# Performance work log

Hardware: AMD Instinct MI355X
Metric: run time of the kernel (lower is better)

Reference implementation:

```python
import jax, jax.numpy as jnp
import numpy as np

B, N, C, K, D, H = 4, 16000, 128, 16, 4, 512
EPS = 1e-5


def _bn(x, g, b, m, v):
    # eval-mode BatchNorm1d over channel dim (applied to flattened B*N rows)
    return (x - m) * jax.lax.rsqrt(v + EPS) * g + b


def _ffn(x, W1, b1, W2, g, b, m, v):
    h = jax.nn.gelu(jnp.einsum('bnc,ch->bnh', x, W1) + b1)
    y = jnp.einsum('bnh,hc->bnc', h, W2)  # second linear has no bias
    return _bn(y, g, b, m, v)


def _vector_feature(x, knn):
    # knn edge max-pooling: max_k ( x[b, knn[b,n,k], :] - x[b, n, :] )
    gathered = jnp.take_along_axis(x[:, :, None, :], knn[:, :, :, None], axis=1)  # (B,N,K,C)
    return jnp.max(gathered - x[:, :, None, :], axis=2)


def _vfr(x, knn, W, g, b, m, v):
    y = jnp.einsum('bnc,cd->bnd', x, W)
    y = _vector_feature(y, knn)
    return _bn(y, g, b, m, v)


def setup_inputs():
    key = jax.random.key(0)
    ks = jax.random.split(key, 16)
    s = 0.05
    return {
        'x': jax.random.normal(ks[0], (B, N, C), jnp.float32),
        'pe': jax.random.normal(ks[1], (B, N, C), jnp.float32),
        'knn': jax.random.randint(ks[2], (B, N, K), 0, N, dtype=jnp.int32),
        # mlp (the single leading FFN)
        'mlp_W1': jax.random.normal(ks[3], (C, H), jnp.float32) * s,
        'mlp_b1': jnp.zeros((H,), jnp.float32),
        'mlp_W2': jax.random.normal(ks[4], (H, C), jnp.float32) * s,
        'mlp_g': jax.random.uniform(ks[5], (C,), jnp.float32, 0.5, 1.5),
        'mlp_beta': jnp.zeros((C,), jnp.float32),
        'mlp_m': jnp.zeros((C,), jnp.float32),
        'mlp_v': jnp.ones((C,), jnp.float32),
        # per-depth VFR params (stacked over depth D)
        'vfr_W': jax.random.normal(ks[6], (D, C, C), jnp.float32) * s,
        'vfr_g': jax.random.uniform(ks[7], (D, C), jnp.float32, 0.5, 1.5),
        'vfr_beta': jnp.zeros((D, C), jnp.float32),
        'vfr_m': jnp.zeros((D, C), jnp.float32),
        'vfr_v': jnp.ones((D, C), jnp.float32),
        # per-depth FFN params
        'ffn_W1': jax.random.normal(ks[8], (D, C, H), jnp.float32) * s,
        'ffn_b1': jnp.zeros((D, H), jnp.float32),
        'ffn_W2': jax.random.normal(ks[9], (D, H, C), jnp.float32) * s,
        'ffn_g': jax.random.uniform(ks[10], (D, C), jnp.float32, 0.5, 1.5),
        'ffn_beta': jnp.zeros((D, C), jnp.float32),
        'ffn_m': jnp.zeros((D, C), jnp.float32),
        'ffn_v': jnp.ones((D, C), jnp.float32),
    }


def reference(x, pe, knn,
              mlp_W1, mlp_b1, mlp_W2, mlp_g, mlp_beta, mlp_m, mlp_v,
              vfr_W, vfr_g, vfr_beta, vfr_m, vfr_v,
              ffn_W1, ffn_b1, ffn_W2, ffn_g, ffn_beta, ffn_m, ffn_v):
    # drop_path is identity in eval mode
    x = x + _ffn(x, mlp_W1, mlp_b1, mlp_W2, mlp_g, mlp_beta, mlp_m, mlp_v)
    for i in range(D):
        x = x + pe
        x = x + _vfr(x, knn, vfr_W[i], vfr_g[i], vfr_beta[i], vfr_m[i], vfr_v[i])
        x = x + _ffn(x, ffn_W1[i], ffn_b1[i], ffn_W2[i], ffn_g[i], ffn_beta[i], ffn_m[i], ffn_v[i])
    return x
```

## Files before the change

kernel.cpp:

```cpp
#include <hip/hip_runtime.h>
#include <hip/hip_bf16.h>

typedef __attribute__((ext_vector_type(8))) short bf16x8;
typedef __attribute__((ext_vector_type(4))) float f32x4;

#define B_ 4
#define N_ 16000
#define C_ 128
#define K_ 16
#define D_ 4
#define H_ 512
#define R_ (B_*N_)
#define TM 64
#define EPSV 1e-5f

__device__ __forceinline__ ushort f2bf(float f) {
    uint32_t b = __builtin_bit_cast(uint32_t, f);
    b += 0x7fffu + ((b >> 16) & 1u);
    return (ushort)(b >> 16);
}
__device__ __forceinline__ float bf2f(ushort u) {
    return __builtin_bit_cast(float, (uint32_t)u << 16);
}
__device__ __forceinline__ float gelu_fast(float v) {
    float v2 = v * v;
    float u = v * fmaf(0.0356774081f, v2, 0.7978845608f);
    float e = __expf(-2.0f * u);
    return v * __builtin_amdgcn_rcpf(1.0f + e);
}
__device__ __forceinline__ void gll16(const void* g, void* l) {
    __builtin_amdgcn_global_load_lds(
        (__attribute__((address_space(1))) void*)g,
        (__attribute__((address_space(3))) void*)l, 16, 0, 0);
}

__global__ void prep_kernel(
    const float* __restrict__ mlp_W1, const float* __restrict__ mlp_b1,
    const float* __restrict__ mlp_W2, const float* __restrict__ mlp_g,
    const float* __restrict__ mlp_be, const float* __restrict__ mlp_m,
    const float* __restrict__ mlp_v,
    const float* __restrict__ vfr_W, const float* __restrict__ vfr_g,
    const float* __restrict__ vfr_be, const float* __restrict__ vfr_m,
    const float* __restrict__ vfr_v,
    const float* __restrict__ ffn_W1, const float* __restrict__ ffn_b1,
    const float* __restrict__ ffn_W2, const float* __restrict__ ffn_g,
    const float* __restrict__ ffn_be, const float* __restrict__ ffn_m,
    const float* __restrict__ ffn_v,
    ushort* __restrict__ w1t, ushort* __restrict__ w2t, ushort* __restrict__ wvt,
    float* __restrict__ b1a, float* __restrict__ fs, float* __restrict__ fb,
    float* __restrict__ vs, float* __restrict__ vb)
{
    int i = blockIdx.x * 256 + threadIdx.x;
    const int NW = 5 * H_ * C_;
    if (i < NW) {
        int f = i / (H_*C_), e = i % (H_*C_);
        int h = e / C_, c = e % C_;
        const float* src = (f == 0) ? mlp_W1 : ffn_W1 + (size_t)(f-1)*C_*H_;
        w1t[i] = f2bf(src[(size_t)c*H_ + h]);
        return;
    }
    i -= NW;
    if (i < NW) {
        int f = i / (H_*C_), e = i % (H_*C_);
        int c = e / H_, h = e % H_;
        const float* src = (f == 0) ? mlp_W2 : ffn_W2 + (size_t)(f-1)*H_*C_;
        w2t[i] = f2bf(src[(size_t)h*C_ + c]);
        return;
    }
    i -= NW;
    if (i < D_*C_*C_) {
        int d = i / (C_*C_), e = i % (C_*C_);
        int co = e / C_, k = e % C_;
        wvt[i] = f2bf(vfr_W[(size_t)d*C_*C_ + (size_t)k*C_ + co]);
        return;
    }
    i -= D_*C_*C_;
    if (i < 5*H_) {
        int f = i / H_, h = i % H_;
        b1a[i] = (f == 0) ? mlp_b1[h] : ffn_b1[(f-1)*H_ + h];
        return;
    }
    i -= 5*H_;
    if (i < 5*C_) {
        int f = i / C_, c = i % C_;
        float g  = (f==0) ? mlp_g[c]  : ffn_g[(f-1)*C_ + c];
        float be = (f==0) ? mlp_be[c] : ffn_be[(f-1)*C_ + c];
        float m  = (f==0) ? mlp_m[c]  : ffn_m[(f-1)*C_ + c];
        float v  = (f==0) ? mlp_v[c]  : ffn_v[(f-1)*C_ + c];
        float s = g * rsqrtf(v + EPSV);
        fs[i] = s; fb[i] = be - m * s;
        return;
    }
    i -= 5*C_;
    if (i < D_*C_) {
        float s = vfr_g[i] * rsqrtf(vfr_v[i] + EPSV);
        vs[i] = s; vb[i] = vfr_be[i] - vfr_m[i] * s;
    }
}

__global__ __launch_bounds__(256, 4) void ffn_kernel(
    const float* __restrict__ xin, float* __restrict__ xout,
    const ushort* __restrict__ W1t,
    const ushort* __restrict__ W2t,
    const float* __restrict__ b1,
    const float* __restrict__ bns, const float* __restrict__ bnb)
{
    __shared__ __attribute__((aligned(16))) char lds[16384 + 16384 + 8192];
    char* W1s = lds;
    char* W2s = lds + 16384;
    char* Hs  = lds + 32768;

    const int tid  = threadIdx.x;
    const int m0   = blockIdx.x * TM;
    const int wv   = tid >> 6;
    const int lane = tid & 63;
    const int lr   = lane & 15;
    const int lh   = lane >> 4;

    bf16x8 xa[4];
    {
        const float* xrow = xin + (size_t)(m0 + wv*16 + lr) * C_ + lh*8;
        #pragma unroll
        for (int kk = 0; kk < 4; ++kk) {
            float4 v0 = *(const float4*)(xrow + kk*32);
            float4 v1 = *(const float4*)(xrow + kk*32 + 4);
            bf16x8 pk;
            pk[0]=(short)f2bf(v0.x); pk[1]=(short)f2bf(v0.y);
            pk[2]=(short)f2bf(v0.z); pk[3]=(short)f2bf(v0.w);
            pk[4]=(short)f2bf(v1.x); pk[5]=(short)f2bf(v1.y);
            pk[6]=(short)f2bf(v1.z); pk[7]=(short)f2bf(v1.w);
            xa[kk] = pk;
        }
    }

    f32x4 acc2[8];
    #pragma unroll
    for (int i = 0; i < 8; ++i) acc2[i] = (f32x4){0.f,0.f,0.f,0.f};

    const int q16 = lane >> 4, l16 = lane & 15;
    const int q8  = lane >> 3, l8  = lane & 7;

    for (int hc = 0; hc < 8; ++hc) {
        const int h0 = hc * 64;
        __syncthreads();

        #pragma unroll
        for (int i = 0; i < 4; ++i) {
            int row = wv*16 + i*4 + q16;
            int cb  = l16*16;
            const char* src = (const char*)(W1t + (size_t)(h0 + row) * C_)
                            + (cb ^ ((row&7)<<4));
            gll16(src, W1s + wv*4096 + i*1024);
        }
        #pragma unroll
        for (int i = 0; i < 4; ++i) {
            int row = wv*32 + i*8 + q8;
            int cb  = l8*16;
            const char* src = (const char*)(W2t + (size_t)row * H_ + h0)
                            + (cb ^ ((row&7)<<4));
            gll16(src, W2s + wv*4096 + i*1024);
        }
        __syncthreads();

        f32x4 acc1[4];
        #pragma unroll
        for (int i = 0; i < 4; ++i) acc1[i] = (f32x4){0.f,0.f,0.f,0.f};
        #pragma unroll
        for (int kk = 0; kk < 4; ++kk) {
            int kb = kk*64 + lh*16;
            #pragma unroll
            for (int nf = 0; nf < 4; ++nf) {
                int rb = nf*16 + lr;
                bf16x8 b = *(bf16x8*)(W1s + rb*256 + (kb ^ ((rb&7)<<4)));
                acc1[nf] = __builtin_amdgcn_mfma_f32_16x16x32_bf16(xa[kk], b, acc1[nf], 0, 0, 0);
            }
        }
        #pragma unroll
        for (int nf = 0; nf < 4; ++nf) {
            int col = nf*16 + lr;
            float bias = b1[h0 + col];
            #pragma unroll
            for (int j = 0; j < 4; ++j) {
                int row = wv*16 + lh*4 + j;
                float g = gelu_fast(acc1[nf][j] + bias);
                *(ushort*)(Hs + row*128 + ((col*2) ^ ((row&7)<<4))) = f2bf(g);
            }
        }
        #pragma unroll
        for (int kk = 0; kk < 2; ++kk) {
            int kb = kk*64 + lh*16;
            int ra = wv*16 + lr;
            bf16x8 a = *(bf16x8*)(Hs + ra*128 + (kb ^ ((ra&7)<<4)));
            #pragma unroll
            for (int nf = 0; nf < 8; ++nf) {
                int rb = nf*16 + lr;
                bf16x8 b = *(bf16x8*)(W2s + rb*128 + (kb ^ ((rb&7)<<4)));
                acc2[nf] = __builtin_amdgcn_mfma_f32_16x16x32_bf16(a, b, acc2[nf], 0, 0, 0);
            }
        }
    }

    #pragma unroll
    for (int nf = 0; nf < 8; ++nf) {
        int col = nf*16 + lr;
        float s = bns[col], bb = bnb[col];
        #pragma unroll
        for (int j = 0; j < 4; ++j) {
            int row = m0 + wv*16 + lh*4 + j;
            size_t o = (size_t)row * C_ + col;
            xout[o] = xin[o] + acc2[nf][j] * s + bb;
        }
    }
}

__global__ __launch_bounds__(256, 2) void vfr_gemm_kernel(
    float* __restrict__ x, const float* __restrict__ pe,
    const ushort* __restrict__ Wvt,
    ushort* __restrict__ tout)
{
    __shared__ __attribute__((aligned(16))) char lds[16384 + 32768];
    char* Xs = lds;
    char* Ws = lds + 16384;

    const int tid  = threadIdx.x;
    const int m0   = blockIdx.x * TM;
    const int wv   = tid >> 6;
    const int lane = tid & 63;
    const int lr   = lane & 15;
    const int lh   = lane >> 4;

    #pragma unroll
    for (int it = 0; it < 4; ++it) {
        int idx = it * 2048 + tid * 8;
        int r = idx >> 7, c = idx & 127;
        size_t go = (size_t)(m0 + r) * C_ + c;
        float4 a0 = *(const float4*)(x + go);
        float4 a1 = *(const float4*)(x + go + 4);
        float4 p0 = *(const float4*)(pe + go);
        float4 p1 = *(const float4*)(pe + go + 4);
        a0.x += p0.x; a0.y += p0.y; a0.z += p0.z; a0.w += p0.w;
        a1.x += p1.x; a1.y += p1.y; a1.z += p1.z; a1.w += p1.w;
        *(float4*)(x + go)     = a0;
        *(float4*)(x + go + 4) = a1;
        bf16x8 pk;
        pk[0]=(short)f2bf(a0.x); pk[1]=(short)f2bf(a0.y);
        pk[2]=(short)f2bf(a0.z); pk[3]=(short)f2bf(a0.w);
        pk[4]=(short)f2bf(a1.x); pk[5]=(short)f2bf(a1.y);
        pk[6]=(short)f2bf(a1.z); pk[7]=(short)f2bf(a1.w);
        *(bf16x8*)(Xs + r*256 + ((c*2) ^ ((r&7)<<4))) = pk;
    }
    #pragma unroll
    for (int it = 0; it < 8; ++it) {
        int e = it * 256 + tid;
        int r = e >> 4; int cb = (e & 15) << 4;
        uint4 w = *(const uint4*)((const char*)(Wvt + (size_t)r * C_) + cb);
        *(uint4*)(Ws + r*256 + (cb ^ ((r&7)<<4))) = w;
    }
    __syncthreads();

    f32x4 acc[8];
    #pragma unroll
    for (int i = 0; i < 8; ++i) acc[i] = (f32x4){0.f,0.f,0.f,0.f};
    #pragma unroll
    for (int kk = 0; kk < 4; ++kk) {
        int kb = kk*64 + lh*16;
        int ra = wv*16 + lr;
        bf16x8 a = *(bf16x8*)(Xs + ra*256 + (kb ^ ((ra&7)<<4)));
        #pragma unroll
        for (int nf = 0; nf < 8; ++nf) {
            int rb = nf*16 + lr;
            bf16x8 b = *(bf16x8*)(Ws + rb*256 + (kb ^ ((rb&7)<<4)));
            acc[nf] = __builtin_amdgcn_mfma_f32_16x16x32_bf16(a, b, acc[nf], 0, 0, 0);
        }
    }
    #pragma unroll
    for (int nf = 0; nf < 8; ++nf) {
        int col = nf*16 + lr;
        #pragma unroll
        for (int j = 0; j < 4; ++j) {
            int row = m0 + wv*16 + lh*4 + j;
            tout[(size_t)row * C_ + col] = f2bf(acc[nf][j]);
        }
    }
}

__global__ __launch_bounds__(256) void vfr_gather_kernel(
    float* __restrict__ x, const ushort* __restrict__ t,
    const int* __restrict__ knn,
    const float* __restrict__ s, const float* __restrict__ bb)
{
    const int wv   = threadIdx.x >> 6;
    const int lane = threadIdx.x & 63;
    const int p = blockIdx.x * 4 + wv;
    const int b = p / N_;
    const int base = b * N_;
    const int* kp = knn + (size_t)p * K_;
    const uint* trow = (const uint*)t;

    uint cen = trow[(size_t)p * 64 + lane];
    float c0 = bf2f((ushort)(cen & 0xffffu));
    float c1 = bf2f((ushort)(cen >> 16));
    float m0v = -INFINITY, m1v = -INFINITY;
    #pragma unroll
    for (int k = 0; k < K_; ++k) {
        int idx = kp[k];
        uint g = trow[(size_t)(base + idx) * 64 + lane];
        m0v = fmaxf(m0v, bf2f((ushort)(g & 0xffffu)));
        m1v = fmaxf(m1v, bf2f((ushort)(g >> 16)));
    }
    m0v -= c0; m1v -= c1;

    int c = lane * 2;
    float2 sv = *(const float2*)(s + c);
    float2 bv = *(const float2*)(bb + c);
    size_t o = (size_t)p * C_ + c;
    float2 xv = *(const float2*)(x + o);
    xv.x += m0v * sv.x + bv.x;
    xv.y += m1v * sv.y + bv.y;
    *(float2*)(x + o) = xv;
}

extern "C" void kernel_launch(void* const* d_in, const int* in_sizes, int n_in,
                              void* d_out, int out_size, void* d_ws, size_t ws_size,
                              hipStream_t stream) {
    const float* x      = (const float*)d_in[0];
    const float* pe     = (const float*)d_in[1];
    const int*   knn    = (const int*)d_in[2];
    const float* mlp_W1 = (const float*)d_in[3];
    const float* mlp_b1 = (const float*)d_in[4];
    const float* mlp_W2 = (const float*)d_in[5];
    const float* mlp_g  = (const float*)d_in[6];
    const float* mlp_be = (const float*)d_in[7];
    const float* mlp_m  = (const float*)d_in[8];
    const float* mlp_v  = (const float*)d_in[9];
    const float* vfr_W  = (const float*)d_in[10];
    const float* vfr_g  = (const float*)d_in[11];
    const float* vfr_be = (const float*)d_in[12];
    const float* vfr_m  = (const float*)d_in[13];
    const float* vfr_v  = (const float*)d_in[14];
    const float* ffn_W1 = (const float*)d_in[15];
    const float* ffn_b1 = (const float*)d_in[16];
    const float* ffn_W2 = (const float*)d_in[17];
    const float* ffn_g  = (const float*)d_in[18];
    const float* ffn_be = (const float*)d_in[19];
    const float* ffn_m  = (const float*)d_in[20];
    const float* ffn_v  = (const float*)d_in[21];
    float* out = (float*)d_out;

    char* ws = (char*)d_ws;
    ushort* tbuf = (ushort*)ws;  ws += (size_t)R_ * C_ * 2;
    ushort* w1t  = (ushort*)ws;  ws += (size_t)5 * H_ * C_ * 2;
    ushort* w2t  = (ushort*)ws;  ws += (size_t)5 * C_ * H_ * 2;
    ushort* wvt  = (ushort*)ws;  ws += (size_t)D_ * C_ * C_ * 2;
    float*  b1a  = (float*)ws;   ws += (size_t)5 * H_ * 4;
    float*  fs   = (float*)ws;   ws += (size_t)5 * C_ * 4;
    float*  fb   = (float*)ws;   ws += (size_t)5 * C_ * 4;
    float*  vs   = (float*)ws;   ws += (size_t)D_ * C_ * 4;
    float*  vb   = (float*)ws;   ws += (size_t)D_ * C_ * 4;

    const int prep_items = 2*(5*H_*C_) + D_*C_*C_ + 5*H_ + 5*C_ + D_*C_;
    prep_kernel<<<(prep_items + 255) / 256, 256, 0, stream>>>(
        mlp_W1, mlp_b1, mlp_W2, mlp_g, mlp_be, mlp_m, mlp_v,
        vfr_W, vfr_g, vfr_be, vfr_m, vfr_v,
        ffn_W1, ffn_b1, ffn_W2, ffn_g, ffn_be, ffn_m, ffn_v,
        w1t, w2t, wvt, b1a, fs, fb, vs, vb);

    ffn_kernel<<<R_/TM, 256, 0, stream>>>(x, out, w1t, w2t, b1a, fs, fb);

    for (int d = 0; d < D_; ++d) {
        vfr_gemm_kernel<<<R_/TM, 256, 0, stream>>>(
            out, pe, wvt + (size_t)d * C_ * C_, tbuf);
        vfr_gather_kernel<<<R_/4, 256, 0, stream>>>(
            out, tbuf, knn, vs + d * C_, vb + d * C_);
        ffn_kernel<<<R_/TM, 256, 0, stream>>>(
            out, out,
            w1t + (size_t)(d+1) * H_ * C_, w2t + (size_t)(d+1) * C_ * H_,
            b1a + (d+1) * H_, fs + (d+1) * C_, fb + (d+1) * C_);
    }
}
```

Baseline: 379.2 us.

## Register-resident FFN intermediate, double-buffered weights, fuse pe add into FFN epilogue

The FFN kernel now swaps MFMA operand roles, so the GELU output of the first GEMM lands in registers already laid out as the A operand of the second GEMM. To make that work, W2 is permuted at prep time, which removes the LDS round trip for the hidden activations. Weight chunks are double-buffered with async global-to-LDS loads and blocks grow to 128 rows with 512 threads. The x+pe addition moves from the VFR GEMM prologue into the preceding FFN epilogue, so VFR GEMM only reads x and loads its weights via global_load_lds. The costs are 64KB LDS per block, which limits occupancy, and a more intricate permutation that must exactly match the MFMA fragment layout.

```diff
diff --git a/kernel.cpp b/kernel.cpp
--- a/kernel.cpp
+++ b/kernel.cpp
@@ -2,6 +2,7 @@
 #include <hip/hip_bf16.h>
 
 typedef __attribute__((ext_vector_type(8))) short bf16x8;
+typedef __attribute__((ext_vector_type(4))) short bf16x4;
 typedef __attribute__((ext_vector_type(4))) float f32x4;
 
 #define B_ 4
@@ -11,7 +12,6 @@
 #define D_ 4
 #define H_ 512
 #define R_ (B_*N_)
-#define TM 64
 #define EPSV 1e-5f
 
 __device__ __forceinline__ ushort f2bf(float f) {
@@ -46,7 +46,7 @@
     const float* __restrict__ ffn_W2, const float* __restrict__ ffn_g,
     const float* __restrict__ ffn_be, const float* __restrict__ ffn_m,
     const float* __restrict__ ffn_v,
-    ushort* __restrict__ w1t, ushort* __restrict__ w2t, ushort* __restrict__ wvt,
+    ushort* __restrict__ w1t, ushort* __restrict__ w2p, ushort* __restrict__ wvt,
     float* __restrict__ b1a, float* __restrict__ fs, float* __restrict__ fb,
     float* __restrict__ vs, float* __restrict__ vb)
 {
@@ -62,9 +62,11 @@
     i -= NW;
     if (i < NW) {
         int f = i / (H_*C_), e = i % (H_*C_);
-        int c = e / H_, h = e % H_;
+        int c = e / H_, p = e % H_;
+        int s = p & 31, lam = s >> 3, j = s & 7;
+        int h = (p & ~31) + lam*4 + (j & 3) + ((j >> 2) << 4);
         const float* src = (f == 0) ? mlp_W2 : ffn_W2 + (size_t)(f-1)*H_*C_;
-        w2t[i] = f2bf(src[(size_t)h*C_ + c]);
+        w2p[i] = f2bf(src[(size_t)h*C_ + c]);
         return;
     }
     i -= NW;
@@ -98,26 +100,49 @@
     }
 }
 
-__global__ __launch_bounds__(256, 4) void ffn_kernel(
+template<bool ADD_PE>
+__global__ __launch_bounds__(512, 4) void ffn_kernel(
     const float* __restrict__ xin, float* __restrict__ xout,
+    const float* __restrict__ pe,
     const ushort* __restrict__ W1t,
-    const ushort* __restrict__ W2t,
+    const ushort* __restrict__ W2p,
     const float* __restrict__ b1,
     const float* __restrict__ bns, const float* __restrict__ bnb)
 {
-    __shared__ __attribute__((aligned(16))) char lds[16384 + 16384 + 8192];
-    char* W1s = lds;
-    char* W2s = lds + 16384;
-    char* Hs  = lds + 32768;
+    __shared__ __attribute__((aligned(16))) char lds[65536];
 
     const int tid  = threadIdx.x;
-    const int m0   = blockIdx.x * TM;
+    const int m0   = blockIdx.x * 128;
     const int wv   = tid >> 6;
     const int lane = tid & 63;
     const int lr   = lane & 15;
     const int lh   = lane >> 4;
 
     bf16x8 xa[4];
+
+    auto stageW = [&](int hc, int buf) {
+        char* base = lds + buf * 32768;
+        const int h0 = hc * 64;
+        #pragma unroll
+        for (int i = 0; i < 2; ++i) {
+            int row = i*32 + wv*4 + (lane >> 4);
+            int cb  = (lane & 15) * 16;
+            const char* src = (const char*)(W1t + (size_t)(h0 + row) * C_)
+                            + (cb ^ ((row & 7) << 4));
+            gll16(src, base + i*8192 + wv*1024);
+        }
+        #pragma unroll
+        for (int i = 0; i < 2; ++i) {
+            int row = i*64 + wv*8 + (lane >> 3);
+            int cb  = (lane & 7) * 16;
+            const char* src = (const char*)(W2p + (size_t)row * H_ + h0)
+                            + (cb ^ ((row & 7) << 4));
+            gll16(src, base + 16384 + i*8192 + wv*1024);
+        }
+    };
+
+    stageW(0, 0);
+
     {
         const float* xrow = xin + (size_t)(m0 + wv*16 + lr) * C_ + lh*8;
         #pragma unroll
@@ -137,30 +162,15 @@
     #pragma unroll
     for (int i = 0; i < 8; ++i) acc2[i] = (f32x4){0.f,0.f,0.f,0.f};
 
-    const int q16 = lane >> 4, l16 = lane & 15;
-    const int q8  = lane >> 3, l8  = lane & 7;
+    __syncthreads();
 
     for (int hc = 0; hc < 8; ++hc) {
-        const int h0 = hc * 64;
-        __syncthreads();
-
-        #pragma unroll
-        for (int i = 0; i < 4; ++i) {
-            int row = wv*16 + i*4 + q16;
-            int cb  = l16*16;
-            const char* src = (const char*)(W1t + (size_t)(h0 + row) * C_)
-                            + (cb ^ ((row&7)<<4));
-            gll16(src, W1s + wv*4096 + i*1024);
-        }
-        #pragma unroll
-        for (int i = 0; i < 4; ++i) {
-            int row = wv*32 + i*8 + q8;
-            int cb  = l8*16;
-            const char* src = (const char*)(W2t + (size_t)row * H_ + h0)
-                            + (cb ^ ((row&7)<<4));
-            gll16(src, W2s + wv*4096 + i*1024);
-        }
-        __syncthreads();
+        const int h0  = hc * 64;
+        const int buf = hc & 1;
+        if (hc < 7) stageW(hc + 1, buf ^ 1);
+
+        char* W1s = lds + buf * 32768;
+        char* W2s = W1s + 16384;
 
         f32x4 acc1[4];
         #pragma unroll
@@ -171,33 +181,33 @@
             #pragma unroll
             for (int nf = 0; nf < 4; ++nf) {
                 int rb = nf*16 + lr;
-                bf16x8 b = *(bf16x8*)(W1s + rb*256 + (kb ^ ((rb&7)<<4)));
-                acc1[nf] = __builtin_amdgcn_mfma_f32_16x16x32_bf16(xa[kk], b, acc1[nf], 0, 0, 0);
+                bf16x8 w1 = *(bf16x8*)(W1s + rb*256 + (kb ^ ((rb&7)<<4)));
+                acc1[nf] = __builtin_amdgcn_mfma_f32_16x16x32_bf16(w1, xa[kk], acc1[nf], 0, 0, 0);
             }
         }
+        bf16x4 pa[4];
         #pragma unroll
         for (int nf = 0; nf < 4; ++nf) {
-            int col = nf*16 + lr;
-            float bias = b1[h0 + col];
-            #pragma unroll
-            for (int j = 0; j < 4; ++j) {
-                int row = wv*16 + lh*4 + j;
-                float g = gelu_fast(acc1[nf][j] + bias);
-                *(ushort*)(Hs + row*128 + ((col*2) ^ ((row&7)<<4))) = f2bf(g);
-            }
-        }
-        #pragma unroll
-        for (int kk = 0; kk < 2; ++kk) {
-            int kb = kk*64 + lh*16;
-            int ra = wv*16 + lr;
-            bf16x8 a = *(bf16x8*)(Hs + ra*128 + (kb ^ ((ra&7)<<4)));
+            float4 bias = *(const float4*)(b1 + h0 + nf*16 + lh*4);
+            bf16x4 p;
+            p[0] = (short)f2bf(gelu_fast(acc1[nf][0] + bias.x));
+            p[1] = (short)f2bf(gelu_fast(acc1[nf][1] + bias.y));
+            p[2] = (short)f2bf(gelu_fast(acc1[nf][2] + bias.z));
+            p[3] = (short)f2bf(gelu_fast(acc1[nf][3] + bias.w));
+            pa[nf] = p;
+        }
+        #pragma unroll
+        for (int g = 0; g < 2; ++g) {
+            bf16x8 af = __builtin_shufflevector(pa[2*g], pa[2*g+1], 0,1,2,3,4,5,6,7);
+            int kb = g*64 + lh*16;
             #pragma unroll
             for (int nf = 0; nf < 8; ++nf) {
                 int rb = nf*16 + lr;
-                bf16x8 b = *(bf16x8*)(W2s + rb*128 + (kb ^ ((rb&7)<<4)));
-                acc2[nf] = __builtin_amdgcn_mfma_f32_16x16x32_bf16(a, b, acc2[nf], 0, 0, 0);
+                bf16x8 w2 = *(bf16x8*)(W2s + rb*128 + (kb ^ ((rb&7)<<4)));
+                acc2[nf] = __builtin_amdgcn_mfma_f32_16x16x32_bf16(af, w2, acc2[nf], 0, 0, 0);
             }
         }
+        __syncthreads();
     }
 
     #pragma unroll
@@ -208,53 +218,49 @@
         for (int j = 0; j < 4; ++j) {
             int row = m0 + wv*16 + lh*4 + j;
             size_t o = (size_t)row * C_ + col;
-            xout[o] = xin[o] + acc2[nf][j] * s + bb;
-        }
-    }
-}
-
-__global__ __launch_bounds__(256, 2) void vfr_gemm_kernel(
-    float* __restrict__ x, const float* __restrict__ pe,
+            float base = xin[o] + (ADD_PE ? pe[o] : 0.0f);
+            xout[o] = base + acc2[nf][j] * s + bb;
+        }
+    }
+}
+
+__global__ __launch_bounds__(256, 4) void vfr_gemm_kernel(
+    const float* __restrict__ x,
     const ushort* __restrict__ Wvt,
     ushort* __restrict__ tout)
 {
-    __shared__ __attribute__((aligned(16))) char lds[16384 + 32768];
-    char* Xs = lds;
-    char* Ws = lds + 16384;
+    __shared__ __attribute__((aligned(16))) char Ws[32768];
 
     const int tid  = threadIdx.x;
-    const int m0   = blockIdx.x * TM;
+    const int m0   = blockIdx.x * 64;
     const int wv   = tid >> 6;
     const int lane = tid & 63;
     const int lr   = lane & 15;
     const int lh   = lane >> 4;
 
     #pragma unroll
-    for (int it = 0; it < 4; ++it) {
-        int idx = it * 2048 + tid * 8;
-        int r = idx >> 7, c = idx & 127;
-        size_t go = (size_t)(m0 + r) * C_ + c;
-        float4 a0 = *(const float4*)(x + go);
-        float4 a1 = *(const float4*)(x + go + 4);
-        float4 p0 = *(const float4*)(pe + go);
-        float4 p1 = *(const float4*)(pe + go + 4);
-        a0.x += p0.x; a0.y += p0.y; a0.z += p0.z; a0.w += p0.w;
-        a1.x += p1.x; a1.y += p1.y; a1.z += p1.z; a1.w += p1.w;
-        *(float4*)(x + go)     = a0;
-        *(float4*)(x + go + 4) = a1;
-        bf16x8 pk;
-        pk[0]=(short)f2bf(a0.x); pk[1]=(short)f2bf(a0.y);
-        pk[2]=(short)f2bf(a0.z); pk[3]=(short)f2bf(a0.w);
-        pk[4]=(short)f2bf(a1.x); pk[5]=(short)f2bf(a1.y);
-        pk[6]=(short)f2bf(a1.z); pk[7]=(short)f2bf(a1.w);
-        *(bf16x8*)(Xs + r*256 + ((c*2) ^ ((r&7)<<4))) = pk;
-    }
-    #pragma unroll
-    for (int it = 0; it < 8; ++it) {
-        int e = it * 256 + tid;
-        int r = e >> 4; int cb = (e & 15) << 4;
-        uint4 w = *(const uint4*)((const char*)(Wvt + (size_t)r * C_) + cb);
-        *(uint4*)(Ws + r*256 + (cb ^ ((r&7)<<4))) = w;
+    for (int i = 0; i < 8; ++i) {
+        int row = i*16 + wv*4 + (lane >> 4);
+        int cb  = (lane & 15) * 16;
+        const char* src = (const char*)(Wvt + (size_t)row * C_)
+                        + (cb ^ ((row & 7) << 4));
+        gll16(src, Ws + i*4096 + wv*1024);
+    }
+
+    bf16x8 xa[4];
+    {
+        const float* xrow = x + (size_t)(m0 + wv*16 + lr) * C_ + lh*8;
+        #pragma unroll
+        for (int kk = 0; kk < 4; ++kk) {
+            float4 v0 = *(const float4*)(xrow + kk*32);
+            float4 v1 = *(const float4*)(xrow + kk*32 + 4);
+            bf16x8 pk;
+            pk[0]=(short)f2bf(v0.x); pk[1]=(short)f2bf(v0.y);
+            pk[2]=(short)f2bf(v0.z); pk[3]=(short)f2bf(v0.w);
+            pk[4]=(short)f2bf(v1.x); pk[5]=(short)f2bf(v1.y);
+            pk[6]=(short)f2bf(v1.z); pk[7]=(short)f2bf(v1.w);
+            xa[kk] = pk;
+        }
     }
     __syncthreads();
 
@@ -264,13 +270,11 @@
     #pragma unroll
     for (int kk = 0; kk < 4; ++kk) {
         int kb = kk*64 + lh*16;
-        int ra = wv*16 + lr;
-        bf16x8 a = *(bf16x8*)(Xs + ra*256 + (kb ^ ((ra&7)<<4)));
         #pragma unroll
         for (int nf = 0; nf < 8; ++nf) {
             int rb = nf*16 + lr;
             bf16x8 b = *(bf16x8*)(Ws + rb*256 + (kb ^ ((rb&7)<<4)));
-            acc[nf] = __builtin_amdgcn_mfma_f32_16x16x32_bf16(a, b, acc[nf], 0, 0, 0);
+            acc[nf] = __builtin_amdgcn_mfma_f32_16x16x32_bf16(xa[kk], b, acc[nf], 0, 0, 0);
         }
     }
     #pragma unroll
@@ -350,7 +354,7 @@
     char* ws = (char*)d_ws;
     ushort* tbuf = (ushort*)ws;  ws += (size_t)R_ * C_ * 2;
     ushort* w1t  = (ushort*)ws;  ws += (size_t)5 * H_ * C_ * 2;
-    ushort* w2t  = (ushort*)ws;  ws += (size_t)5 * C_ * H_ * 2;
+    ushort* w2p  = (ushort*)ws;  ws += (size_t)5 * C_ * H_ * 2;
     ushort* wvt  = (ushort*)ws;  ws += (size_t)D_ * C_ * C_ * 2;
     float*  b1a  = (float*)ws;   ws += (size_t)5 * H_ * 4;
     float*  fs   = (float*)ws;   ws += (size_t)5 * C_ * 4;
@@ -363,18 +367,26 @@
         mlp_W1, mlp_b1, mlp_W2, mlp_g, mlp_be, mlp_m, mlp_v,
         vfr_W, vfr_g, vfr_be, vfr_m, vfr_v,
         ffn_W1, ffn_b1, ffn_W2, ffn_g, ffn_be, ffn_m, ffn_v,
-        w1t, w2t, wvt, b1a, fs, fb, vs, vb);
-
-    ffn_kernel<<<R_/TM, 256, 0, stream>>>(x, out, w1t, w2t, b1a, fs, fb);
+        w1t, w2p, wvt, b1a, fs, fb, vs, vb);
+
+    ffn_kernel<true><<<R_/128, 512, 0, stream>>>(
+        x, out, pe, w1t, w2p, b1a, fs, fb);
 
     for (int d = 0; d < D_; ++d) {
-        vfr_gemm_kernel<<<R_/TM, 256, 0, stream>>>(
-            out, pe, wvt + (size_t)d * C_ * C_, tbuf);
+        vfr_gemm_kernel<<<R_/64, 256, 0, stream>>>(
+            out, wvt + (size_t)d * C_ * C_, tbuf);
         vfr_gather_kernel<<<R_/4, 256, 0, stream>>>(
             out, tbuf, knn, vs + d * C_, vb + d * C_);
-        ffn_kernel<<<R_/TM, 256, 0, stream>>>(
-            out, out,
-            w1t + (size_t)(d+1) * H_ * C_, w2t + (size_t)(d+1) * C_ * H_,
-            b1a + (d+1) * H_, fs + (d+1) * C_, fb + (d+1) * C_);
-    }
-}
+        if (d < D_ - 1) {
+            ffn_kernel<true><<<R_/128, 512, 0, stream>>>(
+                out, out, pe,
+                w1t + (size_t)(d+1) * H_ * C_, w2p + (size_t)(d+1) * C_ * H_,
+                b1a + (d+1) * H_, fs + (d+1) * C_, fb + (d+1) * C_);
+        } else {
+            ffn_kernel<false><<<R_/128, 512, 0, stream>>>(
+                out, out, pe,
+                w1t + (size_t)(d+1) * H_ * C_, w2p + (size_t)(d+1) * C_ * H_,
+                b1a + (d+1) * H_, fs + (d+1) * C_, fb + (d+1) * C_);
+        }
+    }
+}
```

After: 366.2 us. 1.04x faster.
